# Performance work log

Hardware: AMD Instinct MI355X
Metric: run time of the kernel (lower is better)

The kernel has to match this reference:

```python
import jax, jax.numpy as jnp
import numpy as np

N, E, G = 50000, 800000, 64
IN, HID, HEADS, OUT = 128, 64, 4, 128
NEG = 0.2  # PyG GATConv default negative_slope


def setup_inputs() -> dict:
    key = jax.random.key(0)
    ks = jax.random.split(key, 12)
    nrm = lambda k, shape, s: (jax.random.normal(k, shape, jnp.float32) * s)
    x = nrm(ks[0], (N, IN), 1.0)
    edge_index = jax.random.randint(ks[1], (2, E), 0, N)
    batch = jnp.sort(jax.random.randint(ks[2], (N,), 0, G))
    W1 = nrm(ks[3], (IN, HEADS * HID), IN ** -0.5)
    a1_src = nrm(ks[4], (HEADS, HID), HID ** -0.5)
    a1_dst = nrm(ks[5], (HEADS, HID), HID ** -0.5)
    b1 = jnp.zeros((HEADS * HID,), jnp.float32)
    W2 = nrm(ks[6], (HEADS * HID, OUT), (HEADS * HID) ** -0.5)
    a2_src = nrm(ks[7], (1, OUT), OUT ** -0.5)
    a2_dst = nrm(ks[8], (1, OUT), OUT ** -0.5)
    b2 = jnp.zeros((OUT,), jnp.float32)
    fc_W = nrm(ks[9], (OUT, OUT), OUT ** -0.5)
    fc_b = jnp.zeros((OUT,), jnp.float32)
    return dict(x=x, edge_index=edge_index, batch=batch, W1=W1, a1_src=a1_src,
                a1_dst=a1_dst, b1=b1, W2=W2, a2_src=a2_src, a2_dst=a2_dst,
                b2=b2, fc_W=fc_W, fc_b=fc_b)


def gat_conv(x, W, a_src, a_dst, b, src, dst, heads):
    n = x.shape[0]
    ch = W.shape[1] // heads
    h = (x @ W).reshape(n, heads, ch)                      # [n, H, C]
    al_s = jnp.einsum('nhc,hc->nh', h, a_src)              # per-node src logits
    al_d = jnp.einsum('nhc,hc->nh', h, a_dst)
    e = al_s[src] + al_d[dst]                              # [E, H]
    e = jnp.where(e > 0, e, NEG * e)                       # LeakyReLU
    # segment softmax over incoming edges of each dst node
    m = jax.lax.stop_gradient(jax.ops.segment_max(e, dst, num_segments=n))
    m = jnp.where(jnp.isfinite(m), m, 0.0)
    ex = jnp.exp(e - m[dst])
    s = jax.ops.segment_sum(ex, dst, num_segments=n)
    alpha = ex / (s[dst] + 1e-16)                          # [E, H]
    out = jax.ops.segment_sum(h[src] * alpha[..., None], dst, num_segments=n)
    return out.reshape(n, heads * ch) + b                  # concat heads + bias


def reference(x, edge_index, batch, W1, a1_src, a1_dst, b1, W2, a2_src, a2_dst, b2, fc_W, fc_b):
    loops = jnp.arange(N, dtype=edge_index.dtype)          # PyG adds self-loops
    src = jnp.concatenate([edge_index[0], loops])
    dst = jnp.concatenate([edge_index[1], loops])
    h = jax.nn.elu(gat_conv(x, W1, a1_src, a1_dst, b1, src, dst, HEADS))
    h = jax.nn.elu(gat_conv(h, W2, a2_src, a2_dst, b2, src, dst, 1))
    sums = jax.ops.segment_sum(h, batch, num_segments=G)
    cnt = jax.ops.segment_sum(jnp.ones((N,), h.dtype), batch, num_segments=G)
    pooled = sums / jnp.maximum(cnt, 1.0)[:, None]         # global mean pool
    return jax.nn.relu(pooled @ fc_W + fc_b)
```

## Files before the change

kernel.cpp:

```cpp
#include <hip/hip_runtime.h>
#include <math.h>

#define N_NODES 50000
#define N_EDGES 800000
#define N_GRAPHS 64
#define NEG 0.2f

typedef unsigned short us;
typedef us us2 __attribute__((ext_vector_type(2)));
typedef us us4 __attribute__((ext_vector_type(4)));
typedef us us8 __attribute__((ext_vector_type(8)));
typedef short bf16x8 __attribute__((ext_vector_type(8)));
typedef float f32x4 __attribute__((ext_vector_type(4)));

__device__ __forceinline__ us bf16rn(float f) {
  unsigned int u = __float_as_uint(f);
  u += 0x7FFFu + ((u >> 16) & 1u);
  return (us)(u >> 16);
}
__device__ __forceinline__ float bf2f(us h) {
  return __uint_as_float(((unsigned int)h) << 16);
}
__device__ __forceinline__ float readlane_f(float v, int l) {
  return __uint_as_float((unsigned)__builtin_amdgcn_readlane(__float_as_uint(v), l));
}

__global__ __launch_bounds__(256) void prep_kernel(
    const float* __restrict__ x, us* __restrict__ xh, us* __restrict__ xl,
    const float* __restrict__ W1, const float* __restrict__ W2,
    us* __restrict__ w1h, us* __restrict__ w1l,
    us* __restrict__ w2h, us* __restrict__ w2l,
    int* __restrict__ cnt, float* __restrict__ psum) {
  int bid = blockIdx.x, t = threadIdx.x;
  if (bid < 6250) {
    int i = bid * 256 + t;
    float4 v = *(const float4*)&x[(size_t)i * 4];
    us h0 = bf16rn(v.x), h1 = bf16rn(v.y), h2 = bf16rn(v.z), h3 = bf16rn(v.w);
    us4 hv = {h0, h1, h2, h3};
    us4 lv = {bf16rn(v.x - bf2f(h0)), bf16rn(v.y - bf2f(h1)),
              bf16rn(v.z - bf2f(h2)), bf16rn(v.w - bf2f(h3))};
    *(us4*)&xh[(size_t)i * 4] = hv;
    *(us4*)&xl[(size_t)i * 4] = lv;
  } else if (bid < 6506) {
    int idx = (bid - 6250) * 256 + t;
    const float* W; us *oh, *ol; int K, N, li;
    if (idx < 128 * 256) { W = W1; oh = w1h; ol = w1l; K = 128; N = 256; li = idx; }
    else { W = W2; oh = w2h; ol = w2l; K = 256; N = 128; li = idx - 128 * 256; }
    int n = li / K, k = li - n * K;
    float f = W[(size_t)k * N + n];
    us h = bf16rn(f);
    oh[li] = h;
    ol[li] = bf16rn(f - bf2f(h));
  } else {
    int i = (bid - 6506) * 256 + t;
    if (i < N_NODES) cnt[i] = 0;
    if (i < N_GRAPHS * 128) psum[i] = 0.f;
  }
}

__global__ __launch_bounds__(256, 2) void gemm_bf16x3(
    const us* __restrict__ Agh, const us* __restrict__ Agl,
    const us* __restrict__ Bth, const us* __restrict__ Btl,
    us* __restrict__ C, int M, int N, int K, int heads,
    const float* __restrict__ a_src, const float* __restrict__ a_dst,
    float* __restrict__ al_s, float* __restrict__ al_d) {
  __shared__ us smem[4][128][40];
  int t = threadIdx.x;
  int m0 = blockIdx.x * 128;
  int n0 = blockIdx.y * 128;
  int w = t >> 6, l = t & 63;
  int wr = w >> 1, wc = w & 1;
  int l15 = l & 15, g = l >> 4;

  f32x4 acc[4][4] = {};

  for (int kb = 0; kb < K; kb += 32) {
    us8 z = {};
    #pragma unroll
    for (int i = 0; i < 2; i++) {
      int slot = i * 256 + t;
      int row = slot >> 2, kq = slot & 3;
      size_t gi = (size_t)(m0 + row) * K + kb + kq * 8;
      bool ok = (m0 + row) < M;
      *(us8*)&smem[0][row][kq * 8] = ok ? *(const us8*)&Agh[gi] : z;
      *(us8*)&smem[1][row][kq * 8] = ok ? *(const us8*)&Agl[gi] : z;
    }
    #pragma unroll
    for (int i = 0; i < 2; i++) {
      int slot = i * 256 + t;
      int n = slot >> 2, kq = slot & 3;
      size_t gi = (size_t)(n0 + n) * K + kb + kq * 8;
      *(us8*)&smem[2][n][kq * 8] = *(const us8*)&Bth[gi];
      *(us8*)&smem[3][n][kq * 8] = *(const us8*)&Btl[gi];
    }
    __syncthreads();

    bf16x8 af[4], al4[4], bf[4], bl4[4];
    #pragma unroll
    for (int i = 0; i < 4; i++) {
      af[i]  = *(const bf16x8*)&smem[0][wr * 64 + i * 16 + l15][g * 8];
      al4[i] = *(const bf16x8*)&smem[1][wr * 64 + i * 16 + l15][g * 8];
      bf[i]  = *(const bf16x8*)&smem[2][wc * 64 + i * 16 + l15][g * 8];
      bl4[i] = *(const bf16x8*)&smem[3][wc * 64 + i * 16 + l15][g * 8];
    }
    #pragma unroll
    for (int i = 0; i < 4; i++)
      #pragma unroll
      for (int j = 0; j < 4; j++) {
        acc[i][j] = __builtin_amdgcn_mfma_f32_16x16x32_bf16(af[i], bf[j], acc[i][j], 0, 0, 0);
        acc[i][j] = __builtin_amdgcn_mfma_f32_16x16x32_bf16(af[i], bl4[j], acc[i][j], 0, 0, 0);
        acc[i][j] = __builtin_amdgcn_mfma_f32_16x16x32_bf16(al4[i], bf[j], acc[i][j], 0, 0, 0);
      }
    __syncthreads();
  }

  us* ct = &smem[0][0][0];
  #pragma unroll
  for (int i = 0; i < 4; i++)
    #pragma unroll
    for (int j = 0; j < 4; j++)
      #pragma unroll
      for (int r = 0; r < 4; r++) {
        int row = wr * 64 + i * 16 + g * 4 + r;
        int col = wc * 64 + j * 16 + l15;
        ct[row * 128 + col] = bf16rn(acc[i][j][r]);
      }
  __syncthreads();
  #pragma unroll
  for (int q = 0; q < 8; q++) {
    int slot = q * 256 + t;
    int row = slot >> 4, col8 = slot & 15;
    if (m0 + row < M) {
      us8 v = *(const us8*)&ct[row * 128 + col8 * 8];
      *(us8*)&C[(size_t)(m0 + row) * N + n0 + col8 * 8] = v;
    }
  }

  if (heads == 4) {
    int r = t & 127, hs = t >> 7;
    int row = m0 + r;
    if (row < M) {
      int head = blockIdx.y * 2 + hs;
      const float* as = &a_src[head * 64];
      const float* ad = &a_dst[head * 64];
      float ss = 0.f, sd = 0.f;
      #pragma unroll
      for (int k8 = 0; k8 < 8; k8++) {
        us8 v = *(const us8*)&ct[r * 128 + hs * 64 + k8 * 8];
        #pragma unroll
        for (int j = 0; j < 8; j++) {
          float f = bf2f(v[j]);
          ss += f * as[k8 * 8 + j];
          sd += f * ad[k8 * 8 + j];
        }
      }
      al_s[row * 4 + head] = ss;
      al_d[row * 4 + head] = sd;
    }
  } else if (heads == 1) {
    if (t < 128) {
      int row = m0 + t;
      if (row < M) {
        float ss = 0.f, sd = 0.f;
        #pragma unroll
        for (int k8 = 0; k8 < 16; k8++) {
          us8 v = *(const us8*)&ct[t * 128 + k8 * 8];
          #pragma unroll
          for (int j = 0; j < 8; j++) {
            float f = bf2f(v[j]);
            ss += f * a_src[k8 * 8 + j];
            sd += f * a_dst[k8 * 8 + j];
          }
        }
        al_s[row] = ss;
        al_d[row] = sd;
      }
    }
  }
}

__global__ __launch_bounds__(256) void count_kernel(const int* __restrict__ dst,
                                                    int* __restrict__ cnt) {
  int e = blockIdx.x * 256 + threadIdx.x;
  if (e < N_EDGES) atomicAdd(&cnt[dst[e]], 1);
}

__global__ __launch_bounds__(256) void scan1_kernel(const int* __restrict__ cnt,
                                                    int* __restrict__ itmp,
                                                    int* __restrict__ bsum) {
  int i = blockIdx.x * 256 + threadIdx.x;
  int v = (i < N_NODES) ? cnt[i] : 0;
  int lane = threadIdx.x & 63, w = threadIdx.x >> 6;
  int s = v;
  #pragma unroll
  for (int off = 1; off < 64; off <<= 1) {
    int tv = __shfl_up(s, off);
    if (lane >= off) s += tv;
  }
  __shared__ int wsum[4];
  if (lane == 63) wsum[w] = s;
  __syncthreads();
  int add = 0;
  for (int p = 0; p < w; p++) add += wsum[p];
  s += add;
  if (i < N_NODES) itmp[i] = s;
  if (threadIdx.x == 255) bsum[blockIdx.x] = s;
}

__global__ __launch_bounds__(256) void scan3_kernel(const int* __restrict__ cnt,
                                                    const int* __restrict__ itmp,
                                                    const int* __restrict__ bsum,
                                                    int* __restrict__ rowst,
                                                    int* __restrict__ cursor,
                                                    int nb) {
  int t = threadIdx.x;
  int lane = t & 63, w = t >> 6;
  int v = (t < nb && t < blockIdx.x) ? bsum[t] : 0;
  int s = v;
  #pragma unroll
  for (int off = 1; off < 64; off <<= 1) s += __shfl_xor(s, off);
  __shared__ int partial[4];
  if (lane == 0) partial[w] = s;
  __syncthreads();
  int boff = partial[0] + partial[1] + partial[2] + partial[3];
  int i = blockIdx.x * 256 + t;
  if (i < N_NODES) {
    int excl = itmp[i] - cnt[i] + boff;
    rowst[i] = excl;
    cursor[i] = excl;
  }
  if (i == 0) rowst[N_NODES] = N_EDGES;
}

__global__ __launch_bounds__(256) void scatter_kernel(
    const int* __restrict__ src, const int* __restrict__ dst,
    int* __restrict__ cursor, int* __restrict__ csr_src) {
  int e = blockIdx.x * 256 + threadIdx.x;
  if (e < N_EDGES) {
    int p = atomicAdd(&cursor[dst[e]], 1);
    csr_src[p] = src[e];
  }
}

__global__ __launch_bounds__(256) void agg1_kernel(
    const us* __restrict__ h1b, const float* __restrict__ al_s,
    const float* __restrict__ al_d, const int* __restrict__ rowst,
    const int* __restrict__ csrc, const float* __restrict__ b1,
    us* __restrict__ outh, us* __restrict__ outl) {
  int d = (blockIdx.x * 256 + threadIdx.x) >> 6;
  int lane = threadIdx.x & 63;
  if (d >= N_NODES) return;
  int head = lane >> 4;
  int c0 = lane * 4;
  int wsel = lane & 48;
  float ald = al_d[d * 4 + head];
  float wsum = 0.f, a0 = 0.f, a1 = 0.f, a2 = 0.f, a3 = 0.f;
  {
    float v = al_s[d * 4 + head] + ald;
    v = v > 0.f ? v : NEG * v;
    float w = __expf(v);
    us4 hv = *(const us4*)&h1b[(size_t)d * 256 + c0];
    wsum += w;
    a0 += w * bf2f(hv[0]); a1 += w * bf2f(hv[1]);
    a2 += w * bf2f(hv[2]); a3 += w * bf2f(hv[3]);
  }
  int beg = rowst[d], end = rowst[d + 1];
  int j = beg;
  for (; j + 16 <= end; j += 16) {
    int el = lane & 15;
    int sv = csrc[j + el];
    float v = al_s[sv * 4 + head] + ald;
    v = v > 0.f ? v : NEG * v;
    float wv = __expf(v);
    #pragma unroll
    for (int q = 0; q < 16; q += 4) {
      int s0 = __builtin_amdgcn_readlane(sv, q + 0);
      int s1 = __builtin_amdgcn_readlane(sv, q + 1);
      int s2 = __builtin_amdgcn_readlane(sv, q + 2);
      int s3 = __builtin_amdgcn_readlane(sv, q + 3);
      us4 h0 = *(const us4*)&h1b[(size_t)(unsigned)s0 * 256 + c0];
      us4 h1 = *(const us4*)&h1b[(size_t)(unsigned)s1 * 256 + c0];
      us4 h2 = *(const us4*)&h1b[(size_t)(unsigned)s2 * 256 + c0];
      us4 h3 = *(const us4*)&h1b[(size_t)(unsigned)s3 * 256 + c0];
      float w0 = __shfl(wv, q + 0 + wsel);
      float w1 = __shfl(wv, q + 1 + wsel);
      float w2 = __shfl(wv, q + 2 + wsel);
      float w3 = __shfl(wv, q + 3 + wsel);
      wsum += w0 + w1 + w2 + w3;
      a0 += w0 * bf2f(h0[0]) + w1 * bf2f(h1[0]) + w2 * bf2f(h2[0]) + w3 * bf2f(h3[0]);
      a1 += w0 * bf2f(h0[1]) + w1 * bf2f(h1[1]) + w2 * bf2f(h2[1]) + w3 * bf2f(h3[1]);
      a2 += w0 * bf2f(h0[2]) + w1 * bf2f(h1[2]) + w2 * bf2f(h2[2]) + w3 * bf2f(h3[2]);
      a3 += w0 * bf2f(h0[3]) + w1 * bf2f(h1[3]) + w2 * bf2f(h2[3]) + w3 * bf2f(h3[3]);
    }
  }
  int m = end - j;
  if (m > 0) {
    int el = lane & 15;
    int sv = csrc[j + (el < m ? el : 0)];
    float v = al_s[sv * 4 + head] + ald;
    v = v > 0.f ? v : NEG * v;
    float wv = __expf(v);
    for (int q = 0; q < m; q += 4) {
      int k0 = q, k1 = q + 1 < m ? q + 1 : 0, k2 = q + 2 < m ? q + 2 : 0,
          k3 = q + 3 < m ? q + 3 : 0;
      int s0 = __builtin_amdgcn_readlane(sv, k0);
      int s1 = __builtin_amdgcn_readlane(sv, k1);
      int s2 = __builtin_amdgcn_readlane(sv, k2);
      int s3 = __builtin_amdgcn_readlane(sv, k3);
      us4 h0 = *(const us4*)&h1b[(size_t)(unsigned)s0 * 256 + c0];
      us4 h1 = *(const us4*)&h1b[(size_t)(unsigned)s1 * 256 + c0];
      us4 h2 = *(const us4*)&h1b[(size_t)(unsigned)s2 * 256 + c0];
      us4 h3 = *(const us4*)&h1b[(size_t)(unsigned)s3 * 256 + c0];
      float w0 = __shfl(wv, k0 + wsel);
      float w1 = __shfl(wv, k1 + wsel);
      float w2 = __shfl(wv, k2 + wsel);
      float w3 = __shfl(wv, k3 + wsel);
      if (q + 1 >= m) w1 = 0.f;
      if (q + 2 >= m) w2 = 0.f;
      if (q + 3 >= m) w3 = 0.f;
      wsum += w0 + w1 + w2 + w3;
      a0 += w0 * bf2f(h0[0]) + w1 * bf2f(h1[0]) + w2 * bf2f(h2[0]) + w3 * bf2f(h3[0]);
      a1 += w0 * bf2f(h0[1]) + w1 * bf2f(h1[1]) + w2 * bf2f(h2[1]) + w3 * bf2f(h3[1]);
      a2 += w0 * bf2f(h0[2]) + w1 * bf2f(h1[2]) + w2 * bf2f(h2[2]) + w3 * bf2f(h3[2]);
      a3 += w0 * bf2f(h0[3]) + w1 * bf2f(h1[3]) + w2 * bf2f(h2[3]) + w3 * bf2f(h3[3]);
    }
  }
  float inv = 1.f / (wsum + 1e-16f);
  float4 bb = *(const float4*)&b1[c0];
  float o[4] = {a0 * inv + bb.x, a1 * inv + bb.y, a2 * inv + bb.z, a3 * inv + bb.w};
  us4 oh, ol;
  #pragma unroll
  for (int i = 0; i < 4; i++) {
    float e = o[i] > 0.f ? o[i] : expm1f(o[i]);
    us h = bf16rn(e);
    oh[i] = h;
    ol[i] = bf16rn(e - bf2f(h));
  }
  *(us4*)&outh[(size_t)d * 256 + c0] = oh;
  *(us4*)&outl[(size_t)d * 256 + c0] = ol;
}

__global__ __launch_bounds__(256) void agg2_kernel(
    const us* __restrict__ h2b, const float* __restrict__ al_s,
    const float* __restrict__ al_d, const int* __restrict__ rowst,
    const int* __restrict__ csrc, const float* __restrict__ b2,
    float* __restrict__ out) {
  int d = (blockIdx.x * 256 + threadIdx.x) >> 6;
  int lane = threadIdx.x & 63;
  if (d >= N_NODES) return;
  int c0 = lane * 2;
  float ald = al_d[d];
  float wsum = 0.f, a0 = 0.f, a1 = 0.f;
  {
    float v = al_s[d] + ald;
    v = v > 0.f ? v : NEG * v;
    float w = __expf(v);
    us2 hv = *(const us2*)&h2b[(size_t)d * 128 + c0];
    wsum += w;
    a0 += w * bf2f(hv[0]); a1 += w * bf2f(hv[1]);
  }
  int beg = rowst[d], end = rowst[d + 1];
  int j = beg;
  for (; j + 64 <= end; j += 64) {
    int sv = csrc[j + lane];
    float v = al_s[sv] + ald;
    v = v > 0.f ? v : NEG * v;
    float wv = __expf(v);
    for (int q = 0; q < 64; q += 4) {
      int s0 = __builtin_amdgcn_readlane(sv, q + 0);
      int s1 = __builtin_amdgcn_readlane(sv, q + 1);
      int s2 = __builtin_amdgcn_readlane(sv, q + 2);
      int s3 = __builtin_amdgcn_readlane(sv, q + 3);
      us2 h0 = *(const us2*)&h2b[(size_t)(unsigned)s0 * 128 + c0];
      us2 h1 = *(const us2*)&h2b[(size_t)(unsigned)s1 * 128 + c0];
      us2 h2 = *(const us2*)&h2b[(size_t)(unsigned)s2 * 128 + c0];
      us2 h3 = *(const us2*)&h2b[(size_t)(unsigned)s3 * 128 + c0];
      float w0 = readlane_f(wv, q + 0);
      float w1 = readlane_f(wv, q + 1);
      float w2 = readlane_f(wv, q + 2);
      float w3 = readlane_f(wv, q + 3);
      wsum += w0 + w1 + w2 + w3;
      a0 += w0 * bf2f(h0[0]) + w1 * bf2f(h1[0]) + w2 * bf2f(h2[0]) + w3 * bf2f(h3[0]);
      a1 += w0 * bf2f(h0[1]) + w1 * bf2f(h1[1]) + w2 * bf2f(h2[1]) + w3 * bf2f(h3[1]);
    }
  }
  int m = end - j;
  if (m > 0) {
    int sv = csrc[j + (lane < m ? lane : 0)];
    float v = al_s[sv] + ald;
    v = v > 0.f ? v : NEG * v;
    float wv = __expf(v);
    for (int q = 0; q < m; q += 4) {
      int k0 = q, k1 = q + 1 < m ? q + 1 : 0, k2 = q + 2 < m ? q + 2 : 0,
          k3 = q + 3 < m ? q + 3 : 0;
      int s0 = __builtin_amdgcn_readlane(sv, k0);
      int s1 = __builtin_amdgcn_readlane(sv, k1);
      int s2 = __builtin_amdgcn_readlane(sv, k2);
      int s3 = __builtin_amdgcn_readlane(sv, k3);
      us2 h0 = *(const us2*)&h2b[(size_t)(unsigned)s0 * 128 + c0];
      us2 h1 = *(const us2*)&h2b[(size_t)(unsigned)s1 * 128 + c0];
      us2 h2 = *(const us2*)&h2b[(size_t)(unsigned)s2 * 128 + c0];
      us2 h3 = *(const us2*)&h2b[(size_t)(unsigned)s3 * 128 + c0];
      float w0 = readlane_f(wv, k0);
      float w1 = readlane_f(wv, k1);
      float w2 = readlane_f(wv, k2);
      float w3 = readlane_f(wv, k3);
      if (q + 1 >= m) w1 = 0.f;
      if (q + 2 >= m) w2 = 0.f;
      if (q + 3 >= m) w3 = 0.f;
      wsum += w0 + w1 + w2 + w3;
      a0 += w0 * bf2f(h0[0]) + w1 * bf2f(h1[0]) + w2 * bf2f(h2[0]) + w3 * bf2f(h3[0]);
      a1 += w0 * bf2f(h0[1]) + w1 * bf2f(h1[1]) + w2 * bf2f(h2[1]) + w3 * bf2f(h3[1]);
    }
  }
  float inv = 1.f / (wsum + 1e-16f);
  float2 bb = *(const float2*)&b2[c0];
  float o0 = a0 * inv + bb.x, o1 = a1 * inv + bb.y;
  o0 = o0 > 0.f ? o0 : expm1f(o0);
  o1 = o1 > 0.f ? o1 : expm1f(o1);
  *(float2*)&out[(size_t)d * 128 + c0] = make_float2(o0, o1);
}

#define PNPB 128
__global__ __launch_bounds__(256) void pool_kernel(const float* __restrict__ y,
                                                   const int* __restrict__ batch,
                                                   float* __restrict__ psum) {
  int t = threadIdx.x;
  int lane32 = t & 31;
  int sub = t >> 5;
  int base = blockIdx.x * PNPB + sub * (PNPB / 8);
  int nend = base + PNPB / 8;
  if (nend > N_NODES) nend = N_NODES;
  float4 acc = make_float4(0.f, 0.f, 0.f, 0.f);
  int curg = -1;
  for (int n = base; n < nend; ++n) {
    int g = batch[n];
    if (g != curg) {
      if (curg >= 0) {
        float* p = &psum[curg * 128 + lane32 * 4];
        atomicAdd(p + 0, acc.x); atomicAdd(p + 1, acc.y);
        atomicAdd(p + 2, acc.z); atomicAdd(p + 3, acc.w);
      }
      acc = make_float4(0.f, 0.f, 0.f, 0.f);
      curg = g;
    }
    float4 v = *(const float4*)&y[(size_t)n * 128 + lane32 * 4];
    acc.x += v.x; acc.y += v.y; acc.z += v.z; acc.w += v.w;
  }
  if (curg >= 0) {
    float* p = &psum[curg * 128 + lane32 * 4];
    atomicAdd(p + 0, acc.x); atomicAdd(p + 1, acc.y);
    atomicAdd(p + 2, acc.z); atomicAdd(p + 3, acc.w);
  }
}

__global__ __launch_bounds__(128) void fc_kernel(
    const float* __restrict__ psum, const int* __restrict__ batch,
    const float* __restrict__ fcW, const float* __restrict__ fcb,
    float* __restrict__ out) {
  __shared__ float pr[128];
  __shared__ int bounds[2];
  int g = blockIdx.x, c = threadIdx.x;
  if (c < 2) {
    int target = g + c;
    int lo = 0, hi = N_NODES;
    while (lo < hi) {
      int mid = (lo + hi) >> 1;
      if (batch[mid] < target) lo = mid + 1; else hi = mid;
    }
    bounds[c] = lo;
  }
  __syncthreads();
  float cnt = (float)(bounds[1] - bounds[0]);
  cnt = cnt > 1.f ? cnt : 1.f;
  pr[c] = psum[g * 128 + c] / cnt;
  __syncthreads();
  float s = fcb[c];
  #pragma unroll 8
  for (int k = 0; k < 128; k++) s += pr[k] * fcW[k * 128 + c];
  out[g * 128 + c] = fmaxf(s, 0.f);
}

extern "C" void kernel_launch(void* const* d_in, const int* in_sizes, int n_in,
                              void* d_out, int out_size, void* d_ws,
                              size_t ws_size, hipStream_t stream) {
  const float* x      = (const float*)d_in[0];
  const int*   ei     = (const int*)d_in[1];
  const int*   batch  = (const int*)d_in[2];
  const float* W1     = (const float*)d_in[3];
  const float* a1_src = (const float*)d_in[4];
  const float* a1_dst = (const float*)d_in[5];
  const float* b1     = (const float*)d_in[6];
  const float* W2     = (const float*)d_in[7];
  const float* a2_src = (const float*)d_in[8];
  const float* a2_dst = (const float*)d_in[9];
  const float* b2     = (const float*)d_in[10];
  const float* fc_W   = (const float*)d_in[11];
  const float* fc_b   = (const float*)d_in[12];
  float* out = (float*)d_out;

  const int* srcp = ei;
  const int* dstp = ei + N_EDGES;
  const int NB = (N_NODES + 255) / 256;

  float* y    = (float*)d_ws;
  float* al1s = y + (size_t)N_NODES * 128;
  float* al1d = al1s + N_NODES * 4;
  float* al2s = al1d + N_NODES * 4;
  float* al2d = al2s + N_NODES;
  float* psum = al2d + N_NODES;
  us* xh   = (us*)(psum + N_GRAPHS * 128);
  us* xl   = xh + (size_t)N_NODES * 128;
  us* x2h  = xl + (size_t)N_NODES * 128;
  us* x2l  = x2h + (size_t)N_NODES * 256;
  us* h1b  = x2l + (size_t)N_NODES * 256;
  us* h2b  = h1b + (size_t)N_NODES * 256;
  us* w1th = h2b + (size_t)N_NODES * 128;
  us* w1tl = w1th + 256 * 128;
  us* w2th = w1tl + 256 * 128;
  us* w2tl = w2th + 128 * 256;
  int* cnt    = (int*)(w2tl + 128 * 256);
  int* bsum   = cnt + N_NODES;
  int* boff   = bsum + 256;
  int* itmp   = boff + 256;
  int* rowst  = itmp + N_NODES;
  int* cursor = rowst + N_NODES + 8;
  int* csrc   = cursor + N_NODES;
  size_t needed = (size_t)((char*)(csrc + N_EDGES) - (char*)d_ws);
  if (ws_size < needed) return;

  prep_kernel<<<6702, 256, 0, stream>>>(x, xh, xl, W1, W2, w1th, w1tl, w2th,
                                        w2tl, cnt, psum);

  count_kernel<<<(N_EDGES + 255) / 256, 256, 0, stream>>>(dstp, cnt);
  scan1_kernel<<<NB, 256, 0, stream>>>(cnt, itmp, bsum);
  scan3_kernel<<<NB, 256, 0, stream>>>(cnt, itmp, bsum, rowst, cursor, NB);
  scatter_kernel<<<(N_EDGES + 255) / 256, 256, 0, stream>>>(srcp, dstp, cursor, csrc);

  gemm_bf16x3<<<dim3(391, 2), 256, 0, stream>>>(xh, xl, w1th, w1tl, h1b,
                                                N_NODES, 256, 128, 4, a1_src,
                                                a1_dst, al1s, al1d);
  agg1_kernel<<<(N_NODES * 64 + 255) / 256, 256, 0, stream>>>(
      h1b, al1s, al1d, rowst, csrc, b1, x2h, x2l);

  gemm_bf16x3<<<dim3(391, 1), 256, 0, stream>>>(x2h, x2l, w2th, w2tl, h2b,
                                                N_NODES, 128, 256, 1, a2_src,
                                                a2_dst, al2s, al2d);
  agg2_kernel<<<(N_NODES * 64 + 255) / 256, 256, 0, stream>>>(
      h2b, al2s, al2d, rowst, csrc, b2, y);

  pool_kernel<<<(N_NODES + PNPB - 1) / PNPB, 256, 0, stream>>>(y, batch, psum);
  fc_kernel<<<N_GRAPHS, 128, 0, stream>>>(psum, batch, fc_W, fc_b, out);
}
```

Before: 281.9 us.

## Co-schedule layer-1 GEMM with CSR scatter and fuse mean-pool into agg2

Merges the first GEMM and the CSR scatter into one launch, with block indices partitioned between the two so that the independent work runs concurrently. It also fuses global mean pooling into agg2: each block reduces its four node outputs in shared memory and atomically adds them to per-graph sums. This removes the fp32 intermediate node-feature buffer and the separate pool kernel. The cost is many more atomics on psum, one per block per channel instead of one per run of nodes, plus an extra __syncthreads in agg2 and a redundant al_s store.

Result: no change. 283.9 us (+0.7%).

```diff
diff --git a/kernel.cpp b/kernel.cpp
--- a/kernel.cpp
+++ b/kernel.cpp
@@ -5,6 +5,7 @@
 #define N_EDGES 800000
 #define N_GRAPHS 64
 #define NEG 0.2f
+#define GEMM1_BLOCKS 782
 
 typedef unsigned short us;
 typedef us us2 __attribute__((ext_vector_type(2)));
@@ -58,16 +59,16 @@
   }
 }
 
-__global__ __launch_bounds__(256, 2) void gemm_bf16x3(
-    const us* __restrict__ Agh, const us* __restrict__ Agl,
+__device__ __forceinline__ void gemm_body(
+    int bx, int by, const us* __restrict__ Agh, const us* __restrict__ Agl,
     const us* __restrict__ Bth, const us* __restrict__ Btl,
     us* __restrict__ C, int M, int N, int K, int heads,
     const float* __restrict__ a_src, const float* __restrict__ a_dst,
     float* __restrict__ al_s, float* __restrict__ al_d) {
   __shared__ us smem[4][128][40];
   int t = threadIdx.x;
-  int m0 = blockIdx.x * 128;
-  int n0 = blockIdx.y * 128;
+  int m0 = bx * 128;
+  int n0 = by * 128;
   int w = t >> 6, l = t & 63;
   int wr = w >> 1, wc = w & 1;
   int l15 = l & 15, g = l >> 4;
@@ -140,7 +141,7 @@
     int r = t & 127, hs = t >> 7;
     int row = m0 + r;
     if (row < M) {
-      int head = blockIdx.y * 2 + hs;
+      int head = by * 2 + hs;
       const float* as = &a_src[head * 64];
       const float* ad = &a_dst[head * 64];
       float ss = 0.f, sd = 0.f;
@@ -172,9 +173,40 @@
             sd += f * a_dst[k8 * 8 + j];
           }
         }
+        al_s[t == 0 ? row : row] = ss;
         al_s[row] = ss;
         al_d[row] = sd;
       }
+    }
+  }
+}
+
+__global__ __launch_bounds__(256, 2) void gemm_bf16x3(
+    const us* __restrict__ Agh, const us* __restrict__ Agl,
+    const us* __restrict__ Bth, const us* __restrict__ Btl,
+    us* __restrict__ C, int M, int N, int K, int heads,
+    const float* __restrict__ a_src, const float* __restrict__ a_dst,
+    float* __restrict__ al_s, float* __restrict__ al_d) {
+  gemm_body(blockIdx.x, blockIdx.y, Agh, Agl, Bth, Btl, C, M, N, K, heads,
+            a_src, a_dst, al_s, al_d);
+}
+
+__global__ __launch_bounds__(256, 2) void sg_kernel(
+    const us* __restrict__ Agh, const us* __restrict__ Agl,
+    const us* __restrict__ Bth, const us* __restrict__ Btl,
+    us* __restrict__ C,
+    const float* __restrict__ a_src, const float* __restrict__ a_dst,
+    float* __restrict__ al_s, float* __restrict__ al_d,
+    const int* __restrict__ src, const int* __restrict__ dst,
+    int* __restrict__ cursor, int* __restrict__ csr_src) {
+  if (blockIdx.x < GEMM1_BLOCKS) {
+    gemm_body(blockIdx.x % 391, blockIdx.x / 391, Agh, Agl, Bth, Btl, C,
+              N_NODES, 256, 128, 4, a_src, a_dst, al_s, al_d);
+  } else {
+    int e = (blockIdx.x - GEMM1_BLOCKS) * 256 + threadIdx.x;
+    if (e < N_EDGES) {
+      int p = atomicAdd(&cursor[dst[e]], 1);
+      csr_src[p] = src[e];
     }
   }
 }
@@ -230,16 +262,6 @@
     cursor[i] = excl;
   }
   if (i == 0) rowst[N_NODES] = N_EDGES;
-}
-
-__global__ __launch_bounds__(256) void scatter_kernel(
-    const int* __restrict__ src, const int* __restrict__ dst,
-    int* __restrict__ cursor, int* __restrict__ csr_src) {
-  int e = blockIdx.x * 256 + threadIdx.x;
-  if (e < N_EDGES) {
-    int p = atomicAdd(&cursor[dst[e]], 1);
-    csr_src[p] = src[e];
-  }
 }
 
 __global__ __launch_bounds__(256) void agg1_kernel(
@@ -344,113 +366,107 @@
     const us* __restrict__ h2b, const float* __restrict__ al_s,
     const float* __restrict__ al_d, const int* __restrict__ rowst,
     const int* __restrict__ csrc, const float* __restrict__ b2,
-    float* __restrict__ out) {
+    const int* __restrict__ batch, float* __restrict__ psum) {
   int d = (blockIdx.x * 256 + threadIdx.x) >> 6;
   int lane = threadIdx.x & 63;
-  if (d >= N_NODES) return;
+  int wv4 = threadIdx.x >> 6;
   int c0 = lane * 2;
-  float ald = al_d[d];
-  float wsum = 0.f, a0 = 0.f, a1 = 0.f;
-  {
-    float v = al_s[d] + ald;
-    v = v > 0.f ? v : NEG * v;
-    float w = __expf(v);
-    us2 hv = *(const us2*)&h2b[(size_t)d * 128 + c0];
-    wsum += w;
-    a0 += w * bf2f(hv[0]); a1 += w * bf2f(hv[1]);
-  }
-  int beg = rowst[d], end = rowst[d + 1];
-  int j = beg;
-  for (; j + 64 <= end; j += 64) {
-    int sv = csrc[j + lane];
-    float v = al_s[sv] + ald;
-    v = v > 0.f ? v : NEG * v;
-    float wv = __expf(v);
-    for (int q = 0; q < 64; q += 4) {
-      int s0 = __builtin_amdgcn_readlane(sv, q + 0);
-      int s1 = __builtin_amdgcn_readlane(sv, q + 1);
-      int s2 = __builtin_amdgcn_readlane(sv, q + 2);
-      int s3 = __builtin_amdgcn_readlane(sv, q + 3);
-      us2 h0 = *(const us2*)&h2b[(size_t)(unsigned)s0 * 128 + c0];
-      us2 h1 = *(const us2*)&h2b[(size_t)(unsigned)s1 * 128 + c0];
-      us2 h2 = *(const us2*)&h2b[(size_t)(unsigned)s2 * 128 + c0];
-      us2 h3 = *(const us2*)&h2b[(size_t)(unsigned)s3 * 128 + c0];
-      float w0 = readlane_f(wv, q + 0);
-      float w1 = readlane_f(wv, q + 1);
-      float w2 = readlane_f(wv, q + 2);
-      float w3 = readlane_f(wv, q + 3);
-      wsum += w0 + w1 + w2 + w3;
-      a0 += w0 * bf2f(h0[0]) + w1 * bf2f(h1[0]) + w2 * bf2f(h2[0]) + w3 * bf2f(h3[0]);
-      a1 += w0 * bf2f(h0[1]) + w1 * bf2f(h1[1]) + w2 * bf2f(h2[1]) + w3 * bf2f(h3[1]);
-    }
-  }
-  int m = end - j;
-  if (m > 0) {
-    int sv = csrc[j + (lane < m ? lane : 0)];
-    float v = al_s[sv] + ald;
-    v = v > 0.f ? v : NEG * v;
-    float wv = __expf(v);
-    for (int q = 0; q < m; q += 4) {
-      int k0 = q, k1 = q + 1 < m ? q + 1 : 0, k2 = q + 2 < m ? q + 2 : 0,
-          k3 = q + 3 < m ? q + 3 : 0;
-      int s0 = __builtin_amdgcn_readlane(sv, k0);
-      int s1 = __builtin_amdgcn_readlane(sv, k1);
-      int s2 = __builtin_amdgcn_readlane(sv, k2);
-      int s3 = __builtin_amdgcn_readlane(sv, k3);
-      us2 h0 = *(const us2*)&h2b[(size_t)(unsigned)s0 * 128 + c0];
-      us2 h1 = *(const us2*)&h2b[(size_t)(unsigned)s1 * 128 + c0];
-      us2 h2 = *(const us2*)&h2b[(size_t)(unsigned)s2 * 128 + c0];
-      us2 h3 = *(const us2*)&h2b[(size_t)(unsigned)s3 * 128 + c0];
-      float w0 = readlane_f(wv, k0);
-      float w1 = readlane_f(wv, k1);
-      float w2 = readlane_f(wv, k2);
-      float w3 = readlane_f(wv, k3);
-      if (q + 1 >= m) w1 = 0.f;
-      if (q + 2 >= m) w2 = 0.f;
-      if (q + 3 >= m) w3 = 0.f;
-      wsum += w0 + w1 + w2 + w3;
-      a0 += w0 * bf2f(h0[0]) + w1 * bf2f(h1[0]) + w2 * bf2f(h2[0]) + w3 * bf2f(h3[0]);
-      a1 += w0 * bf2f(h0[1]) + w1 * bf2f(h1[1]) + w2 * bf2f(h2[1]) + w3 * bf2f(h3[1]);
-    }
-  }
-  float inv = 1.f / (wsum + 1e-16f);
-  float2 bb = *(const float2*)&b2[c0];
-  float o0 = a0 * inv + bb.x, o1 = a1 * inv + bb.y;
-  o0 = o0 > 0.f ? o0 : expm1f(o0);
-  o1 = o1 > 0.f ? o1 : expm1f(o1);
-  *(float2*)&out[(size_t)d * 128 + c0] = make_float2(o0, o1);
-}
-
-#define PNPB 128
-__global__ __launch_bounds__(256) void pool_kernel(const float* __restrict__ y,
-                                                   const int* __restrict__ batch,
-                                                   float* __restrict__ psum) {
+  bool valid = d < N_NODES;
+  float o0 = 0.f, o1 = 0.f;
+  if (valid) {
+    float ald = al_d[d];
+    float wsum = 0.f, a0 = 0.f, a1 = 0.f;
+    {
+      float v = al_s[d] + ald;
+      v = v > 0.f ? v : NEG * v;
+      float w = __expf(v);
+      us2 hv = *(const us2*)&h2b[(size_t)d * 128 + c0];
+      wsum += w;
+      a0 += w * bf2f(hv[0]); a1 += w * bf2f(hv[1]);
+    }
+    int beg = rowst[d], end = rowst[d + 1];
+    int j = beg;
+    for (; j + 64 <= end; j += 64) {
+      int sv = csrc[j + lane];
+      float v = al_s[sv] + ald;
+      v = v > 0.f ? v : NEG * v;
+      float wvv = __expf(v);
+      for (int q = 0; q < 64; q += 4) {
+        int s0 = __builtin_amdgcn_readlane(sv, q + 0);
+        int s1 = __builtin_amdgcn_readlane(sv, q + 1);
+        int s2 = __builtin_amdgcn_readlane(sv, q + 2);
+        int s3 = __builtin_amdgcn_readlane(sv, q + 3);
+        us2 h0 = *(const us2*)&h2b[(size_t)(unsigned)s0 * 128 + c0];
+        us2 h1 = *(const us2*)&h2b[(size_t)(unsigned)s1 * 128 + c0];
+        us2 h2 = *(const us2*)&h2b[(size_t)(unsigned)s2 * 128 + c0];
+        us2 h3 = *(const us2*)&h2b[(size_t)(unsigned)s3 * 128 + c0];
+        float w0 = readlane_f(wvv, q + 0);
+        float w1 = readlane_f(wvv, q + 1);
+        float w2 = readlane_f(wvv, q + 2);
+        float w3 = readlane_f(wvv, q + 3);
+        wsum += w0 + w1 + w2 + w3;
+        a0 += w0 * bf2f(h0[0]) + w1 * bf2f(h1[0]) + w2 * bf2f(h2[0]) + w3 * bf2f(h3[0]);
+        a1 += w0 * bf2f(h0[1]) + w1 * bf2f(h1[1]) + w2 * bf2f(h2[1]) + w3 * bf2f(h3[1]);
+      }
+    }
+    int m = end - j;
+    if (m > 0) {
+      int sv = csrc[j + (lane < m ? lane : 0)];
+      float v = al_s[sv] + ald;
+      v = v > 0.f ? v : NEG * v;
+      float wvv = __expf(v);
+      for (int q = 0; q < m; q += 4) {
+        int k0 = q, k1 = q + 1 < m ? q + 1 : 0, k2 = q + 2 < m ? q + 2 : 0,
+            k3 = q + 3 < m ? q + 3 : 0;
+        int s0 = __builtin_amdgcn_readlane(sv, k0);
+        int s1 = __builtin_amdgcn_readlane(sv, k1);
+        int s2 = __builtin_amdgcn_readlane(sv, k2);
+        int s3 = __builtin_amdgcn_readlane(sv, k3);
+        us2 h0 = *(const us2*)&h2b[(size_t)(unsigned)s0 * 128 + c0];
+        us2 h1 = *(const us2*)&h2b[(size_t)(unsigned)s1 * 128 + c0];
+        us2 h2 = *(const us2*)&h2b[(size_t)(unsigned)s2 * 128 + c0];
+        us2 h3 = *(const us2*)&h2b[(size_t)(unsigned)s3 * 128 + c0];
+        float w0 = readlane_f(wvv, k0);
+        float w1 = readlane_f(wvv, k1);
+        float w2 = readlane_f(wvv, k2);
+        float w3 = readlane_f(wvv, k3);
+        if (q + 1 >= m) w1 = 0.f;
+        if (q + 2 >= m) w2 = 0.f;
+        if (q + 3 >= m) w3 = 0.f;
+        wsum += w0 + w1 + w2 + w3;
+        a0 += w0 * bf2f(h0[0]) + w1 * bf2f(h1[0]) + w2 * bf2f(h2[0]) + w3 * bf2f(h3[0]);
+        a1 += w0 * bf2f(h0[1]) + w1 * bf2f(h1[1]) + w2 * bf2f(h2[1]) + w3 * bf2f(h3[1]);
+      }
+    }
+    float inv = 1.f / (wsum + 1e-16f);
+    float2 bb = *(const float2*)&b2[c0];
+    o0 = a0 * inv + bb.x;
+    o1 = a1 * inv + bb.y;
+    o0 = o0 > 0.f ? o0 : expm1f(o0);
+    o1 = o1 > 0.f ? o1 : expm1f(o1);
+  }
+  __shared__ float sh[4][128];
+  __shared__ int sg[4];
+  sh[wv4][c0] = o0;
+  sh[wv4][c0 + 1] = o1;
+  if (lane == 0) sg[wv4] = valid ? batch[d] : -1;
+  __syncthreads();
   int t = threadIdx.x;
-  int lane32 = t & 31;
-  int sub = t >> 5;
-  int base = blockIdx.x * PNPB + sub * (PNPB / 8);
-  int nend = base + PNPB / 8;
-  if (nend > N_NODES) nend = N_NODES;
-  float4 acc = make_float4(0.f, 0.f, 0.f, 0.f);
-  int curg = -1;
-  for (int n = base; n < nend; ++n) {
-    int g = batch[n];
-    if (g != curg) {
-      if (curg >= 0) {
-        float* p = &psum[curg * 128 + lane32 * 4];
-        atomicAdd(p + 0, acc.x); atomicAdd(p + 1, acc.y);
-        atomicAdd(p + 2, acc.z); atomicAdd(p + 3, acc.w);
-      }
-      acc = make_float4(0.f, 0.f, 0.f, 0.f);
-      curg = g;
-    }
-    float4 v = *(const float4*)&y[(size_t)n * 128 + lane32 * 4];
-    acc.x += v.x; acc.y += v.y; acc.z += v.z; acc.w += v.w;
-  }
-  if (curg >= 0) {
-    float* p = &psum[curg * 128 + lane32 * 4];
-    atomicAdd(p + 0, acc.x); atomicAdd(p + 1, acc.y);
-    atomicAdd(p + 2, acc.z); atomicAdd(p + 3, acc.w);
+  if (t < 128) {
+    int cur = -1;
+    float accv = 0.f;
+    #pragma unroll
+    for (int ww = 0; ww < 4; ++ww) {
+      int g = sg[ww];
+      if (g < 0) continue;
+      if (g != cur) {
+        if (cur >= 0) atomicAdd(&psum[cur * 128 + t], accv);
+        cur = g;
+        accv = 0.f;
+      }
+      accv += sh[ww][t];
+    }
+    if (cur >= 0) atomicAdd(&psum[cur * 128 + t], accv);
   }
 }
 
@@ -503,8 +519,7 @@
   const int* dstp = ei + N_EDGES;
   const int NB = (N_NODES + 255) / 256;
 
-  float* y    = (float*)d_ws;
-  float* al1s = y + (size_t)N_NODES * 128;
+  float* al1s = (float*)d_ws;
   float* al1d = al1s + N_NODES * 4;
   float* al2s = al1d + N_NODES * 4;
   float* al2d = al2s + N_NODES;
@@ -521,8 +536,7 @@
   us* w2tl = w2th + 128 * 256;
   int* cnt    = (int*)(w2tl + 128 * 256);
   int* bsum   = cnt + N_NODES;
-  int* boff   = bsum + 256;
-  int* itmp   = boff + 256;
+  int* itmp   = bsum + 256;
   int* rowst  = itmp + N_NODES;
   int* cursor = rowst + N_NODES + 8;
   int* csrc   = cursor + N_NODES;
@@ -535,11 +549,11 @@
   count_kernel<<<(N_EDGES + 255) / 256, 256, 0, stream>>>(dstp, cnt);
   scan1_kernel<<<NB, 256, 0, stream>>>(cnt, itmp, bsum);
   scan3_kernel<<<NB, 256, 0, stream>>>(cnt, itmp, bsum, rowst, cursor, NB);
-  scatter_kernel<<<(N_EDGES + 255) / 256, 256, 0, stream>>>(srcp, dstp, cursor, csrc);
-
-  gemm_bf16x3<<<dim3(391, 2), 256, 0, stream>>>(xh, xl, w1th, w1tl, h1b,
-                                                N_NODES, 256, 128, 4, a1_src,
-                                                a1_dst, al1s, al1d);
+
+  sg_kernel<<<GEMM1_BLOCKS + (N_EDGES + 255) / 256, 256, 0, stream>>>(
+      xh, xl, w1th, w1tl, h1b, a1_src, a1_dst, al1s, al1d,
+      srcp, dstp, cursor, csrc);
+
   agg1_kernel<<<(N_NODES * 64 + 255) / 256, 256, 0, stream>>>(
       h1b, al1s, al1d, rowst, csrc, b1, x2h, x2l);
 
@@ -547,8 +561,7 @@
                                                 N_NODES, 128, 256, 1, a2_src,
                                                 a2_dst, al2s, al2d);
   agg2_kernel<<<(N_NODES * 64 + 255) / 256, 256, 0, stream>>>(
-      h2b, al2s, al2d, rowst, csrc, b2, y);
-
-  pool_kernel<<<(N_NODES + PNPB - 1) / PNPB, 256, 0, stream>>>(y, batch, psum);
+      h2b, al2s, al2d, rowst, csrc, b2, batch, psum);
+
   fc_kernel<<<N_GRAPHS, 128, 0, stream>>>(psum, batch, fc_W, fc_b, out);
 }
```
